# Kernel optimization log

Measured on AMD Instinct MI355X. Metric: run time of the kernel, lower is better.

The kernel has to match this reference:

```python
import jax, jax.numpy as jnp
import numpy as np

H = 16          # num_attention_heads
D = 64          # attention_head_size
BUCKET = 128    # bucket_size
MAX_BUCKETS = 32
TEMP = 0.75
SINKHORN_ITERS = 5
NOISE_KEY = 42  # fixed key for gumbel routing noise (deterministic reference)


def _sinkhorn_route(pl, W, key):
    # pl: [b,h,buckets,d] bucket summaries, W: [h,d,buckets]
    R = jnp.einsum('bhid,hdf->bhif', pl, W)  # [b,h,buckets,buckets]
    u = jax.random.uniform(key, R.shape, R.dtype)
    gumbel = -jnp.log(-jnp.log(u + 1e-6) + 1e-6)
    R = (R + gumbel) / TEMP
    for _ in range(SINKHORN_ITERS):
        R = R - jax.scipy.special.logsumexp(R, axis=-1, keepdims=True)
        R = R - jax.scipy.special.logsumexp(R, axis=-2, keepdims=True)
    return jnp.exp(R)


def setup_inputs() -> dict:
    key = jax.random.key(0)
    kq, kk, kv, kwk, kwv = jax.random.split(key, 5)
    q = jax.random.normal(kq, (64, 4096, 64), jnp.float32)
    k = jax.random.normal(kk, (64, 4096, 64), jnp.float32)
    v = jax.random.normal(kv, (64, 4096, 64), jnp.float32)
    W_keys = jax.random.normal(kwk, (H, D, MAX_BUCKETS), jnp.float32)
    W_vals = jax.random.normal(kwv, (H, D, MAX_BUCKETS), jnp.float32)
    return {'q': q, 'k': k, 'v': v, 'W_keys': W_keys, 'W_vals': W_vals}


def reference(q, q_unused=None, *, _=None, **__):
    raise RuntimeError  # placeholder, replaced below


def reference(q, k, v, W_keys, W_vals):
    t, d = q.shape[1], q.shape[2]
    buckets = t // BUCKET
    # [b, h, buckets, bucket_size, d]
    b_q = q.reshape(-1, H, buckets, BUCKET, d)
    b_k = k.reshape(-1, H, buckets, BUCKET, d)
    b_v = v.reshape(-1, H, buckets, BUCKET, d)

    pl_k = b_k.sum(axis=-2)  # [b,h,buckets,d]
    R_k = _sinkhorn_route(pl_k, W_keys[..., :buckets], jax.random.key(NOISE_KEY))
    # NOTE: original also computes R_v / b_v_r but never uses them for output.

    b_k = jnp.einsum('bhij,bhjsd->bhisd', R_k, b_k) + b_k

    dots = jnp.einsum('bhuid,bhujd->bhuij', b_q, b_k) * (d ** -0.5)
    probs = jax.nn.softmax(dots, axis=-1)
    out = jnp.einsum('bhuij,bhujd->bhuid', probs, b_v)  # [b,h,buckets,s,d]
    return out.reshape(-1, t, d)
```

## Files before the change

kernel.cpp:

```cpp
#include <hip/hip_runtime.h>
#include <math.h>

#define BH 64
#define NB 32
#define BS 128
#define DHEAD 64

typedef __attribute__((ext_vector_type(8))) short bf16x8;
typedef __attribute__((ext_vector_type(4))) float f32x4;

#define LDK 72
#define LDV 76
#define LDP 136

__device__ __forceinline__ unsigned rotl32(unsigned x, int d) {
    return (x << d) | (x >> (32 - d));
}

__device__ __forceinline__ void threefry2x32(unsigned k0, unsigned k1,
                                             unsigned& x0, unsigned& x1) {
    const unsigned ks0 = k0, ks1 = k1, ks2 = k0 ^ k1 ^ 0x1BD11BDAu;
    const int r0[4] = {13, 15, 26, 6};
    const int r1[4] = {17, 29, 16, 24};
    x0 += ks0; x1 += ks1;
    #pragma unroll
    for (int i = 0; i < 4; i++) { x0 += x1; x1 = rotl32(x1, r0[i]); x1 ^= x0; }
    x0 += ks1; x1 += ks2 + 1u;
    #pragma unroll
    for (int i = 0; i < 4; i++) { x0 += x1; x1 = rotl32(x1, r1[i]); x1 ^= x0; }
    x0 += ks2; x1 += ks0 + 2u;
    #pragma unroll
    for (int i = 0; i < 4; i++) { x0 += x1; x1 = rotl32(x1, r0[i]); x1 ^= x0; }
    x0 += ks0; x1 += ks1 + 3u;
    #pragma unroll
    for (int i = 0; i < 4; i++) { x0 += x1; x1 = rotl32(x1, r1[i]); x1 ^= x0; }
    x0 += ks1; x1 += ks2 + 4u;
    #pragma unroll
    for (int i = 0; i < 4; i++) { x0 += x1; x1 = rotl32(x1, r0[i]); x1 ^= x0; }
    x0 += ks2; x1 += ks0 + 5u;
}

__device__ __forceinline__ float jax_uniform_part(unsigned f) {
    unsigned x0 = 0u, x1 = f;
    threefry2x32(0u, 42u, x0, x1);
    unsigned bits = x0 ^ x1;
    return __uint_as_float((bits >> 9) | 0x3F800000u) - 1.0f;
}

__global__ void __launch_bounds__(256)
pl_kernel(const float* __restrict__ k, float* __restrict__ pl) {
    int blk = blockIdx.x;
    int g = threadIdx.x >> 6;
    int d = threadIdx.x & 63;
    const float* kp = k + (size_t)blk * 8192 + (size_t)g * 2048 + d;
    float s = 0.f;
    #pragma unroll
    for (int i = 0; i < 32; i++) s += kp[i * 64];
    __shared__ float red[4][64];
    red[g][d] = s;
    __syncthreads();
    if (threadIdx.x < 64)
        pl[blk * 64 + threadIdx.x] = (red[0][threadIdx.x] + red[1][threadIdx.x])
                                   + (red[2][threadIdx.x] + red[3][threadIdx.x]);
}

__global__ void route_kernel(const float* __restrict__ pl, const float* __restrict__ Wk,
                             float* __restrict__ Rout) {
    int bh = blockIdx.x;
    int h = bh & 15;
    int tid = threadIdx.x;
    int i = tid >> 5, j = tid & 31;

    __shared__ float plS[NB * DHEAD];
    __shared__ float T[32 * 33];
    __shared__ float colL[32];

    for (int x = tid; x < NB * DHEAD; x += 1024) plS[x] = pl[bh * NB * DHEAD + x];
    __syncthreads();

    float acc = 0.f;
    #pragma unroll 8
    for (int d2 = 0; d2 < DHEAD; d2++)
        acc += plS[i * DHEAD + d2] * Wk[(h * DHEAD + d2) * NB + j];

    unsigned f = (unsigned)bh * 1024u + (unsigned)i * 32u + (unsigned)j;
    float u = jax_uniform_part(f);
    float g = -logf(-logf(u + 1e-6f) + 1e-6f);
    float val = (acc + g) / 0.75f;

    for (int it = 0; it < 5; it++) {
        float m = val;
        #pragma unroll
        for (int off = 1; off < 32; off <<= 1) m = fmaxf(m, __shfl_xor(m, off, 32));
        float s = expf(val - m);
        #pragma unroll
        for (int off = 1; off < 32; off <<= 1) s += __shfl_xor(s, off, 32);
        val -= m + logf(s);

        T[i * 33 + j] = val;
        __syncthreads();
        float tv = T[j * 33 + i];
        float m2 = tv;
        #pragma unroll
        for (int off = 1; off < 32; off <<= 1) m2 = fmaxf(m2, __shfl_xor(m2, off, 32));
        float s2 = expf(tv - m2);
        #pragma unroll
        for (int off = 1; off < 32; off <<= 1) s2 += __shfl_xor(s2, off, 32);
        if (j == 0) colL[i] = m2 + logf(s2);
        __syncthreads();
        val -= colL[j];
    }
    Rout[bh * 1024 + i * 32 + j] = expf(val) + (i == j ? 1.0f : 0.0f);
}

__global__ void __launch_bounds__(256)
mix_kernel(const float* __restrict__ k, const float* __restrict__ Rp,
           float* __restrict__ Kp) {
    __shared__ float X[32][260];
    int bh = blockIdx.x >> 5;
    int tile = blockIdx.x & 31;
    const size_t kbase = (size_t)bh * 262144;
    const int col0 = tile * 256;

    {
        int j = threadIdx.x >> 3;
        int cs = (threadIdx.x & 7) * 32;
        const float4* src = (const float4*)(k + kbase + (size_t)j * 8192 + col0 + cs);
        #pragma unroll
        for (int t = 0; t < 8; t++)
            *((float4*)&X[j][cs + 4 * t]) = src[t];
    }
    __syncthreads();

    const int col = threadIdx.x;
    float xv[32];
    #pragma unroll
    for (int j = 0; j < 32; j++) xv[j] = X[j][col];

    const float* Rb = Rp + bh * 1024;
    float* outp = Kp + kbase + col0 + col;
    #pragma unroll 4
    for (int i = 0; i < 32; i++) {
        float acc = 0.f;
        #pragma unroll
        for (int j = 0; j < 32; j++) acc = fmaf(Rb[i * 32 + j], xv[j], acc);
        outp[(size_t)i * 8192] = acc;
    }
}

__global__ void __launch_bounds__(256)
attn_mfma_kernel(const float* __restrict__ q, const float* __restrict__ Kp,
                 const float* __restrict__ v, float* __restrict__ out) {
    __shared__ __align__(16) unsigned short smem[2 * 128 * LDK + 128 * LDV];
    unsigned short* KhS = smem;
    unsigned short* KlS = smem + 128 * LDK;
    unsigned short* VbS = smem + 256 * LDK;
    unsigned short* PbS = smem;

    const int tid = threadIdx.x;
    const int w = tid >> 6, lane = tid & 63;
    const int quad = lane >> 4, l15 = lane & 15;
    const int row0 = 32 * w;
    const size_t base = (size_t)blockIdx.x * (BS * DHEAD);

    bf16x8 qh[2][2], ql[2][2];
    #pragma unroll
    for (int ti = 0; ti < 2; ti++) {
        #pragma unroll
        for (int kk = 0; kk < 2; kk++) {
            const float* qp = q + base + (size_t)(row0 + 16 * ti + l15) * DHEAD
                              + kk * 32 + quad * 8;
            float4 a = ((const float4*)qp)[0];
            float4 b = ((const float4*)qp)[1];
            float f[8] = {a.x, a.y, a.z, a.w, b.x, b.y, b.z, b.w};
            #pragma unroll
            for (int j = 0; j < 8; j++) {
                float qs = f[j] * 0.125f;
                unsigned bits = __float_as_uint(qs);
                unsigned short hi = (unsigned short)(bits >> 16);
                float rem = qs - __uint_as_float(bits & 0xFFFF0000u);
                unsigned short lo = (unsigned short)(__float_as_uint(rem) >> 16);
                qh[ti][kk][j] = (short)hi;
                ql[ti][kk][j] = (short)lo;
            }
        }
    }

    {
        int r = tid >> 1, c0 = (tid & 1) * 32;
        const float* kp = Kp + base + (size_t)r * DHEAD + c0;
        const float* vp = v  + base + (size_t)r * DHEAD + c0;
        #pragma unroll
        for (int x = 0; x < 8; x++) {
            float4 a = ((const float4*)kp)[x];
            float4 b = ((const float4*)vp)[x];
            float kf[4] = {a.x, a.y, a.z, a.w};
            float vf[4] = {b.x, b.y, b.z, b.w};
            #pragma unroll
            for (int y = 0; y < 4; y++) {
                int c = c0 + 4 * x + y;
                unsigned kb = __float_as_uint(kf[y]);
                unsigned short hi = (unsigned short)(kb >> 16);
                float rem = kf[y] - __uint_as_float(kb & 0xFFFF0000u);
                unsigned short lo = (unsigned short)(__float_as_uint(rem) >> 16);
                KhS[r * LDK + c] = hi;
                KlS[r * LDK + c] = lo;
                unsigned vb_ = __float_as_uint(vf[y]);
                VbS[r * LDV + c] = (unsigned short)((vb_ + 0x8000u) >> 16);
            }
        }
    }
    __syncthreads();

    f32x4 acc[2][8];
    #pragma unroll
    for (int ti = 0; ti < 2; ti++)
        #pragma unroll
        for (int tc = 0; tc < 8; tc++)
            acc[ti][tc] = (f32x4){0.f, 0.f, 0.f, 0.f};

    #pragma unroll
    for (int tc = 0; tc < 8; tc++) {
        const int jrow = 16 * tc + l15;
        bf16x8 bh0 = *(const bf16x8*)&KhS[jrow * LDK + 0  + quad * 8];
        bf16x8 bh1 = *(const bf16x8*)&KhS[jrow * LDK + 32 + quad * 8];
        bf16x8 bl0 = *(const bf16x8*)&KlS[jrow * LDK + 0  + quad * 8];
        bf16x8 bl1 = *(const bf16x8*)&KlS[jrow * LDK + 32 + quad * 8];
        #pragma unroll
        for (int ti = 0; ti < 2; ti++) {
            f32x4 c = acc[ti][tc];
            c = __builtin_amdgcn_mfma_f32_16x16x32_bf16(qh[ti][0], bh0, c, 0, 0, 0);
            c = __builtin_amdgcn_mfma_f32_16x16x32_bf16(qh[ti][1], bh1, c, 0, 0, 0);
            c = __builtin_amdgcn_mfma_f32_16x16x32_bf16(ql[ti][0], bh0, c, 0, 0, 0);
            c = __builtin_amdgcn_mfma_f32_16x16x32_bf16(ql[ti][1], bh1, c, 0, 0, 0);
            c = __builtin_amdgcn_mfma_f32_16x16x32_bf16(qh[ti][0], bl0, c, 0, 0, 0);
            c = __builtin_amdgcn_mfma_f32_16x16x32_bf16(qh[ti][1], bl1, c, 0, 0, 0);
            acc[ti][tc] = c;
        }
    }

    float mrow[2][4], lrow[2][4];
    #pragma unroll
    for (int ti = 0; ti < 2; ti++)
        #pragma unroll
        for (int r = 0; r < 4; r++) {
            float m = acc[ti][0][r];
            #pragma unroll
            for (int tc = 1; tc < 8; tc++) m = fmaxf(m, acc[ti][tc][r]);
            #pragma unroll
            for (int off = 1; off < 16; off <<= 1)
                m = fmaxf(m, __shfl_xor(m, off, 64));
            mrow[ti][r] = m;
        }
    #pragma unroll
    for (int ti = 0; ti < 2; ti++)
        #pragma unroll
        for (int r = 0; r < 4; r++) {
            float s = 0.f;
            #pragma unroll
            for (int tc = 0; tc < 8; tc++) {
                float p = __expf(acc[ti][tc][r] - mrow[ti][r]);
                acc[ti][tc][r] = p;
                s += p;
            }
            #pragma unroll
            for (int off = 1; off < 16; off <<= 1)
                s += __shfl_xor(s, off, 64);
            lrow[ti][r] = s;
        }

    __syncthreads();

    #pragma unroll
    for (int ti = 0; ti < 2; ti++)
        #pragma unroll
        for (int tc = 0; tc < 8; tc++)
            #pragma unroll
            for (int r = 0; r < 4; r++) {
                int prow = row0 + 16 * ti + quad * 4 + r;
                unsigned pb = __float_as_uint(acc[ti][tc][r]);
                PbS[prow * LDP + 16 * tc + l15] = (unsigned short)((pb + 0x8000u) >> 16);
            }
    __syncthreads();

    f32x4 oacc[2][4];
    #pragma unroll
    for (int ti = 0; ti < 2; ti++)
        #pragma unroll
        for (int tc = 0; tc < 4; tc++)
            oacc[ti][tc] = (f32x4){0.f, 0.f, 0.f, 0.f};

    #pragma unroll
    for (int kc = 0; kc < 4; kc++) {
        bf16x8 aP[2];
        #pragma unroll
        for (int ti = 0; ti < 2; ti++)
            aP[ti] = *(const bf16x8*)&PbS[(row0 + 16 * ti + l15) * LDP + kc * 32 + quad * 8];
        #pragma unroll
        for (int tc = 0; tc < 4; tc++) {
            bf16x8 vb;
            #pragma unroll
            for (int j = 0; j < 8; j++)
                vb[j] = (short)VbS[(kc * 32 + quad * 8 + j) * LDV + 16 * tc + l15];
            #pragma unroll
            for (int ti = 0; ti < 2; ti++)
                oacc[ti][tc] = __builtin_amdgcn_mfma_f32_16x16x32_bf16(aP[ti], vb, oacc[ti][tc], 0, 0, 0);
        }
    }

    float inv[2][4];
    #pragma unroll
    for (int ti = 0; ti < 2; ti++)
        #pragma unroll
        for (int r = 0; r < 4; r++) inv[ti][r] = 1.0f / lrow[ti][r];

    #pragma unroll
    for (int ti = 0; ti < 2; ti++)
        #pragma unroll
        for (int tc = 0; tc < 4; tc++)
            #pragma unroll
            for (int r = 0; r < 4; r++) {
                int orow = row0 + 16 * ti + quad * 4 + r;
                out[base + (size_t)orow * DHEAD + 16 * tc + l15] = oacc[ti][tc][r] * inv[ti][r];
            }
}

extern "C" void kernel_launch(void* const* d_in, const int* in_sizes, int n_in,
                              void* d_out, int out_size, void* d_ws, size_t ws_size,
                              hipStream_t stream) {
    const float* q  = (const float*)d_in[0];
    const float* k  = (const float*)d_in[1];
    const float* v  = (const float*)d_in[2];
    const float* Wk = (const float*)d_in[3];
    float* out = (float*)d_out;

    float* Kp = (float*)d_ws;
    float* pl = Kp + (size_t)16777216;
    float* R  = pl + (size_t)131072;

    pl_kernel<<<dim3(BH * NB), dim3(256), 0, stream>>>(k, pl);
    route_kernel<<<dim3(BH), dim3(1024), 0, stream>>>(pl, Wk, R);
    mix_kernel<<<dim3(BH * NB), dim3(256), 0, stream>>>(k, R, Kp);
    attn_mfma_kernel<<<dim3(BH * NB), dim3(256), 0, stream>>>(q, Kp, v, out);
}
```

Before: 291.9 us.

## Emit split bf16 K from mix kernel, transpose V in LDS, vectorize pl sums

The mix kernel now writes the mixed keys directly as hi/lo bf16 halves instead of fp32, so the attention kernel copies them into shared memory without doing the split conversion itself. V is packed as bf16 pairs into a transposed LDS layout, so the PV MFMA B operand becomes one vector load instead of eight scalar loads. The bucket-sum kernel switches to float4 loads with a 16-way reduction. The intermediate K traffic stays about the same size (two 2-byte planes instead of one 4-byte array), but the mix kernel now writes with 2-byte stores, which may be less efficient.

```diff
diff --git a/kernel.cpp b/kernel.cpp
--- a/kernel.cpp
+++ b/kernel.cpp
@@ -10,7 +10,7 @@
 typedef __attribute__((ext_vector_type(4))) float f32x4;
 
 #define LDK 72
-#define LDV 76
+#define LDW 68
 #define LDP 136
 
 __device__ __forceinline__ unsigned rotl32(unsigned x, int d) {
@@ -50,18 +50,24 @@
 __global__ void __launch_bounds__(256)
 pl_kernel(const float* __restrict__ k, float* __restrict__ pl) {
     int blk = blockIdx.x;
-    int g = threadIdx.x >> 6;
-    int d = threadIdx.x & 63;
-    const float* kp = k + (size_t)blk * 8192 + (size_t)g * 2048 + d;
-    float s = 0.f;
-    #pragma unroll
-    for (int i = 0; i < 32; i++) s += kp[i * 64];
-    __shared__ float red[4][64];
-    red[g][d] = s;
-    __syncthreads();
-    if (threadIdx.x < 64)
-        pl[blk * 64 + threadIdx.x] = (red[0][threadIdx.x] + red[1][threadIdx.x])
-                                   + (red[2][threadIdx.x] + red[3][threadIdx.x]);
+    int rg = threadIdx.x >> 4;
+    int d4 = (threadIdx.x & 15) * 4;
+    const float* kp = k + (size_t)blk * 8192 + (size_t)rg * 8 * 64 + d4;
+    float4 s = {0.f, 0.f, 0.f, 0.f};
+    #pragma unroll
+    for (int i = 0; i < 8; i++) {
+        float4 t = *(const float4*)(kp + i * 64);
+        s.x += t.x; s.y += t.y; s.z += t.z; s.w += t.w;
+    }
+    __shared__ float red[16][64];
+    *(float4*)&red[rg][d4] = s;
+    __syncthreads();
+    if (threadIdx.x < 64) {
+        float acc = 0.f;
+        #pragma unroll
+        for (int g = 0; g < 16; g++) acc += red[g][threadIdx.x];
+        pl[blk * 64 + threadIdx.x] = acc;
+    }
 }
 
 __global__ void route_kernel(const float* __restrict__ pl, const float* __restrict__ Wk,
@@ -115,7 +121,7 @@
 
 __global__ void __launch_bounds__(256)
 mix_kernel(const float* __restrict__ k, const float* __restrict__ Rp,
-           float* __restrict__ Kp) {
+           unsigned short* __restrict__ Kh, unsigned short* __restrict__ Kl) {
     __shared__ float X[32][260];
     int bh = blockIdx.x >> 5;
     int tile = blockIdx.x & 31;
@@ -138,30 +144,39 @@
     for (int j = 0; j < 32; j++) xv[j] = X[j][col];
 
     const float* Rb = Rp + bh * 1024;
-    float* outp = Kp + kbase + col0 + col;
+    unsigned short* oh = Kh + kbase + col0 + col;
+    unsigned short* ol = Kl + kbase + col0 + col;
     #pragma unroll 4
     for (int i = 0; i < 32; i++) {
         float acc = 0.f;
         #pragma unroll
         for (int j = 0; j < 32; j++) acc = fmaf(Rb[i * 32 + j], xv[j], acc);
-        outp[(size_t)i * 8192] = acc;
+        unsigned kb = __float_as_uint(acc);
+        unsigned short hi = (unsigned short)(kb >> 16);
+        float rem = acc - __uint_as_float(kb & 0xFFFF0000u);
+        unsigned short lo = (unsigned short)(__float_as_uint(rem) >> 16);
+        oh[(size_t)i * 8192] = hi;
+        ol[(size_t)i * 8192] = lo;
     }
 }
 
 __global__ void __launch_bounds__(256)
-attn_mfma_kernel(const float* __restrict__ q, const float* __restrict__ Kp,
+attn_mfma_kernel(const float* __restrict__ q,
+                 const unsigned short* __restrict__ Kh,
+                 const unsigned short* __restrict__ Kl,
                  const float* __restrict__ v, float* __restrict__ out) {
-    __shared__ __align__(16) unsigned short smem[2 * 128 * LDK + 128 * LDV];
-    unsigned short* KhS = smem;
-    unsigned short* KlS = smem + 128 * LDK;
-    unsigned short* VbS = smem + 256 * LDK;
-    unsigned short* PbS = smem;
+    __shared__ __align__(16) unsigned char smem[2 * 128 * LDK * 2 + 64 * LDW * 4];
+    unsigned short* KhS = (unsigned short*)smem;
+    unsigned short* KlS = KhS + 128 * LDK;
+    unsigned*       VT  = (unsigned*)(smem + 2 * 128 * LDK * 2);
+    unsigned short* PbS = (unsigned short*)smem;
 
     const int tid = threadIdx.x;
     const int w = tid >> 6, lane = tid & 63;
     const int quad = lane >> 4, l15 = lane & 15;
     const int row0 = 32 * w;
     const size_t base = (size_t)blockIdx.x * (BS * DHEAD);
+    const size_t base2 = (size_t)blockIdx.x * (BS * DHEAD);
 
     bf16x8 qh[2][2], ql[2][2];
     #pragma unroll
@@ -188,26 +203,33 @@
 
     {
         int r = tid >> 1, c0 = (tid & 1) * 32;
-        const float* kp = Kp + base + (size_t)r * DHEAD + c0;
-        const float* vp = v  + base + (size_t)r * DHEAD + c0;
-        #pragma unroll
-        for (int x = 0; x < 8; x++) {
-            float4 a = ((const float4*)kp)[x];
-            float4 b = ((const float4*)vp)[x];
-            float kf[4] = {a.x, a.y, a.z, a.w};
-            float vf[4] = {b.x, b.y, b.z, b.w};
-            #pragma unroll
-            for (int y = 0; y < 4; y++) {
-                int c = c0 + 4 * x + y;
-                unsigned kb = __float_as_uint(kf[y]);
-                unsigned short hi = (unsigned short)(kb >> 16);
-                float rem = kf[y] - __uint_as_float(kb & 0xFFFF0000u);
-                unsigned short lo = (unsigned short)(__float_as_uint(rem) >> 16);
-                KhS[r * LDK + c] = hi;
-                KlS[r * LDK + c] = lo;
-                unsigned vb_ = __float_as_uint(vf[y]);
-                VbS[r * LDV + c] = (unsigned short)((vb_ + 0x8000u) >> 16);
-            }
+        const unsigned short* khg = Kh + base2 + (size_t)r * 64 + c0;
+        const unsigned short* klg = Kl + base2 + (size_t)r * 64 + c0;
+        #pragma unroll
+        for (int x = 0; x < 4; x++) {
+            bf16x8 th = *(const bf16x8*)(khg + 8 * x);
+            bf16x8 tl = *(const bf16x8*)(klg + 8 * x);
+            *(bf16x8*)&KhS[r * LDK + c0 + 8 * x] = th;
+            *(bf16x8*)&KlS[r * LDK + c0 + 8 * x] = tl;
+        }
+    }
+
+    {
+        int a = tid & 63;
+        int cs = (tid >> 6) * 16;
+        const float* v0p = v + base + (size_t)(2 * a) * 64 + cs;
+        const float* v1p = v0p + 64;
+        float r0[16], r1[16];
+        #pragma unroll
+        for (int t = 0; t < 4; t++) {
+            ((float4*)r0)[t] = ((const float4*)v0p)[t];
+            ((float4*)r1)[t] = ((const float4*)v1p)[t];
+        }
+        #pragma unroll
+        for (int y = 0; y < 16; y++) {
+            unsigned wd = ((__float_as_uint(r0[y]) + 0x8000u) >> 16)
+                        | (((__float_as_uint(r1[y]) + 0x8000u) >> 16) << 16);
+            VT[(cs + y) * LDW + a] = wd;
         }
     }
     __syncthreads();
@@ -298,10 +320,7 @@
             aP[ti] = *(const bf16x8*)&PbS[(row0 + 16 * ti + l15) * LDP + kc * 32 + quad * 8];
         #pragma unroll
         for (int tc = 0; tc < 4; tc++) {
-            bf16x8 vb;
-            #pragma unroll
-            for (int j = 0; j < 8; j++)
-                vb[j] = (short)VbS[(kc * 32 + quad * 8 + j) * LDV + 16 * tc + l15];
+            bf16x8 vb = *(const bf16x8*)&VT[(16 * tc + l15) * LDW + kc * 16 + quad * 4];
             #pragma unroll
             for (int ti = 0; ti < 2; ti++)
                 oacc[ti][tc] = __builtin_amdgcn_mfma_f32_16x16x32_bf16(aP[ti], vb, oacc[ti][tc], 0, 0, 0);
@@ -334,12 +353,13 @@
     const float* Wk = (const float*)d_in[3];
     float* out = (float*)d_out;
 
-    float* Kp = (float*)d_ws;
-    float* pl = Kp + (size_t)16777216;
+    unsigned short* Kh = (unsigned short*)d_ws;
+    unsigned short* Kl = Kh + (size_t)16777216;
+    float* pl = (float*)(Kl + (size_t)16777216);
     float* R  = pl + (size_t)131072;
 
     pl_kernel<<<dim3(BH * NB), dim3(256), 0, stream>>>(k, pl);
     route_kernel<<<dim3(BH), dim3(1024), 0, stream>>>(pl, Wk, R);
-    mix_kernel<<<dim3(BH * NB), dim3(256), 0, stream>>>(k, R, Kp);
-    attn_mfma_kernel<<<dim3(BH * NB), dim3(256), 0, stream>>>(q, Kp, v, out);
-}
+    mix_kernel<<<dim3(BH * NB), dim3(256), 0, stream>>>(k, R, Kh, Kl);
+    attn_mfma_kernel<<<dim3(BH * NB), dim3(256), 0, stream>>>(q, Kh, Kl, v, out);
+}
```

After: 303.1 us. 3.9% more time.
